# Performance work log

Measured on AMD Instinct MI355X. Metric: run time of the kernel, lower is better.

## Reference

```python
import jax, jax.numpy as jnp
import numpy as np

EPS = 1e-10


def _gcn(X, A, W, act):
    # A_hat = A + I; symmetric normalization D^{-1/2} A_hat D^{-1/2}
    N = A.shape[0]
    A_hat = A + jnp.eye(N, dtype=A.dtype)
    d = 1.0 / jnp.sqrt(jnp.sum(A_hat, axis=1) + EPS)
    A_norm = (d[:, None] * A_hat) * d[None, :]  # same math as diag @ A_hat @ diag
    return act(A_norm @ (X @ W))


def _pool(X, A, s, k):
    scores = (X @ s)[:, 0]            # [N]
    _, idx = jax.lax.top_k(scores, k)  # static k (ceil(ratio*N))
    return X[idx], A[idx][:, idx], idx


def _unpool(Xp, idx, N):
    return jnp.zeros((N, Xp.shape[-1]), Xp.dtype).at[idx].set(Xp)


def _glorot(key, shape):
    lim = np.sqrt(6.0 / (shape[0] + shape[1])).astype(np.float32)
    return jax.random.uniform(key, shape, jnp.float32, -lim, lim)


def setup_inputs() -> dict:
    key = jax.random.key(0)
    ks = jax.random.split(key, 8)
    N, F_IN, F, C = 8192, 16, 32, 2
    x = jax.random.normal(ks[0], (N, F_IN), jnp.float32)
    # sparse-ish symmetric binary adjacency stored densely (as the module expects)
    a = (jax.random.uniform(ks[1], (N, N)) < 0.01).astype(jnp.float32)
    a = jnp.maximum(a, a.T)
    return {
        "x": x,
        "a": a,
        "W1": _glorot(ks[2], (F_IN, F)),
        "W2": _glorot(ks[3], (F, F)),
        "W3": _glorot(ks[4], (F, F)),
        "W4": _glorot(ks[5], (F, C)),
        "s1": _glorot(ks[6], (F, 1)),
        "s2": _glorot(ks[7], (F, 1)),
    }


def reference(x, a, W1, W2, W3, W4, s1, s2):
    N = x.shape[0]
    K1 = int(np.ceil(0.5 * N))   # pool1 ratio 0.5
    K2 = int(np.ceil(0.5 * K1))  # pool2 ratio 0.5
    relu = jax.nn.relu
    X1 = _gcn(x, a, W1, relu)                     # [N, F]
    X1p, A1p, idx1 = _pool(X1, a, s1, K1)         # [K1, F], [K1, K1]
    X2 = _gcn(X1p, A1p, W2, relu)                 # [K1, F]
    X2p, _, idx2 = _pool(X2, A1p, s2, K2)         # [K2, F]
    X3 = _unpool(X2p, idx2, K1)                   # scatter back to [K1, F]
    X3 = _gcn(X3, A1p, W3, relu)
    X4 = _unpool(X3, idx1, N)                     # scatter back to [N, F]
    return _gcn(X4, a, W4, lambda z: jax.nn.softmax(z, axis=-1))
```

## Files before the change

### kernel.cpp

```cpp
#include <hip/hip_runtime.h>
#include <stdint.h>

#define NNODES 8192
#define KP1 4096
#define KP2 2048
#define FIN 16
#define FH 32
#define COUT 2
#define STRA 320
#define STRS 320

__global__ __launch_bounds__(256) void build_ell(const float* __restrict__ A, int n, int stride,
        int* __restrict__ ell, int* __restrict__ rowcnt, int* __restrict__ diag, float* __restrict__ dnorm,
        const float* __restrict__ Xf, const float* __restrict__ Wf, float* __restrict__ Zf, int kf)
{
    if ((int)blockIdx.x >= n) {
        int t = ((int)blockIdx.x - n) * 256 + threadIdx.x;
        int i = t >> 5;
        int f = t & 31;
        const float* xr = Xf + (size_t)i * kf;
        float acc = 0.0f;
        for (int k = 0; k < kf; ++k) acc += xr[k] * Wf[k * 32 + f];
        Zf[t] = acc;
        return;
    }
    __shared__ int cnt;
    __shared__ int dg;
    int row = blockIdx.x;
    if (threadIdx.x == 0) { cnt = 0; dg = 0; }
    __syncthreads();
    const float4* arow4 = (const float4*)(A + (size_t)row * n);
    int* erow = ell + (size_t)row * stride;
    int n4 = n >> 2;
    for (int c4 = threadIdx.x; c4 < n4; c4 += 256) {
        float4 v = arow4[c4];
        if (v.x == 0.0f && v.y == 0.0f && v.z == 0.0f && v.w == 0.0f) continue;
        int cb = c4 << 2;
        if (v.x != 0.0f) {
            if (cb == row) dg = 1;
            else { int p = atomicAdd(&cnt, 1); if (p < stride) erow[p] = cb; }
        }
        if (v.y != 0.0f) {
            int c = cb + 1;
            if (c == row) dg = 1;
            else { int p = atomicAdd(&cnt, 1); if (p < stride) erow[p] = c; }
        }
        if (v.z != 0.0f) {
            int c = cb + 2;
            if (c == row) dg = 1;
            else { int p = atomicAdd(&cnt, 1); if (p < stride) erow[p] = c; }
        }
        if (v.w != 0.0f) {
            int c = cb + 3;
            if (c == row) dg = 1;
            else { int p = atomicAdd(&cnt, 1); if (p < stride) erow[p] = c; }
        }
    }
    __syncthreads();
    if (threadIdx.x == 0) {
        int cf = cnt;
        rowcnt[row] = cf < stride ? cf : stride;
        diag[row] = dg;
        dnorm[row] = rsqrtf((float)(cf + dg + 1) + 1e-10f);
    }
}

__global__ __launch_bounds__(256) void spmm_f32(const int* __restrict__ ell, const int* __restrict__ rowcnt,
        const int* __restrict__ diag, const float* __restrict__ dnorm, const float* __restrict__ Z,
        const int* __restrict__ remap, const int* __restrict__ maskp,
        float* __restrict__ X, float* __restrict__ scores, const float* __restrict__ svec,
        const float* __restrict__ W4p, float* __restrict__ z4out,
        int n, int stride)
{
    int wid = (blockIdx.x * 256 + threadIdx.x) >> 6;
    int lane = threadIdx.x & 63;
    if (wid >= n) return;
    int g = lane >> 3;
    int q = lane & 7;
    int cnt = rowcnt[wid];
    const int* erow = ell + (size_t)wid * stride;
    float ax = 0.0f, ay = 0.0f, az = 0.0f, aw = 0.0f;
    for (int it = g; it < cnt; it += 8) {
        int c = erow[it];
        if (maskp && maskp[c] < 0) continue;
        int zc = c;
        if (remap) zc = remap[c];
        float dn = dnorm[c];
        const float4* zp = (const float4*)(Z + (size_t)zc * 32);
        float4 zv = zp[q];
        ax += dn * zv.x;
        ay += dn * zv.y;
        az += dn * zv.z;
        aw += dn * zv.w;
    }
    ax += __shfl_xor(ax, 8);
    ay += __shfl_xor(ay, 8);
    az += __shfl_xor(az, 8);
    aw += __shfl_xor(aw, 8);
    ax += __shfl_xor(ax, 16);
    ay += __shfl_xor(ay, 16);
    az += __shfl_xor(az, 16);
    aw += __shfl_xor(aw, 16);
    ax += __shfl_xor(ax, 32);
    ay += __shfl_xor(ay, 32);
    az += __shfl_xor(az, 32);
    aw += __shfl_xor(aw, 32);
    if (g == 0) {
        float dr = dnorm[wid];
        int selfok = 1;
        if (maskp && maskp[wid] < 0) selfok = 0;
        if (selfok) {
            int zc = wid;
            if (remap) zc = remap[wid];
            const float4* zp = (const float4*)(Z + (size_t)zc * 32);
            float4 zv = zp[q];
            float cf = (float)(diag[wid] + 1) * dr;
            ax += cf * zv.x;
            ay += cf * zv.y;
            az += cf * zv.z;
            aw += cf * zv.w;
        }
        float ox = fmaxf(dr * ax, 0.0f);
        float oy = fmaxf(dr * ay, 0.0f);
        float oz = fmaxf(dr * az, 0.0f);
        float ow = fmaxf(dr * aw, 0.0f);
        if (z4out) {
            int kb = q * 4;
            float p0 = ox * W4p[(kb + 0) * 2 + 0] + oy * W4p[(kb + 1) * 2 + 0]
                     + oz * W4p[(kb + 2) * 2 + 0] + ow * W4p[(kb + 3) * 2 + 0];
            float p1 = ox * W4p[(kb + 0) * 2 + 1] + oy * W4p[(kb + 1) * 2 + 1]
                     + oz * W4p[(kb + 2) * 2 + 1] + ow * W4p[(kb + 3) * 2 + 1];
            p0 += __shfl_xor(p0, 1);
            p1 += __shfl_xor(p1, 1);
            p0 += __shfl_xor(p0, 2);
            p1 += __shfl_xor(p1, 2);
            p0 += __shfl_xor(p0, 4);
            p1 += __shfl_xor(p1, 4);
            if (q == 0) {
                float2 r;
                r.x = p0;
                r.y = p1;
                ((float2*)z4out)[wid] = r;
            }
        } else {
            float4 o;
            o.x = ox; o.y = oy; o.z = oz; o.w = ow;
            float4* xp = (float4*)(X + (size_t)wid * 32);
            xp[q] = o;
            if (scores) {
                const float4* sp = (const float4*)svec;
                float4 sv = sp[q];
                float p = o.x * sv.x + o.y * sv.y + o.z * sv.z + o.w * sv.w;
                p += __shfl_xor(p, 1);
                p += __shfl_xor(p, 2);
                p += __shfl_xor(p, 4);
                if (q == 0) scores[wid] = p;
            }
        }
    }
}

__global__ __launch_bounds__(256) void spmm_out(const int* __restrict__ ell, const int* __restrict__ rowcnt,
        const int* __restrict__ diag, const float* __restrict__ dnorm, const float* __restrict__ Zr,
        const int* __restrict__ gat, float* __restrict__ out, int n, int stride)
{
    int wid = (blockIdx.x * 256 + threadIdx.x) >> 6;
    int lane = threadIdx.x & 63;
    if (wid >= n) return;
    int cnt = rowcnt[wid];
    const int* erow = ell + (size_t)wid * stride;
    const float2* Z2 = (const float2*)Zr;
    float ax = 0.0f, ay = 0.0f;
    for (int it = lane; it < cnt; it += 64) {
        int c = erow[it];
        int rk = gat[c];
        if (rk >= 0) {
            float dn = dnorm[c];
            float2 zv = Z2[rk];
            ax += dn * zv.x;
            ay += dn * zv.y;
        }
    }
    ax += __shfl_xor(ax, 1);
    ay += __shfl_xor(ay, 1);
    ax += __shfl_xor(ax, 2);
    ay += __shfl_xor(ay, 2);
    ax += __shfl_xor(ax, 4);
    ay += __shfl_xor(ay, 4);
    ax += __shfl_xor(ax, 8);
    ay += __shfl_xor(ay, 8);
    ax += __shfl_xor(ax, 16);
    ay += __shfl_xor(ay, 16);
    ax += __shfl_xor(ax, 32);
    ay += __shfl_xor(ay, 32);
    if (lane == 0) {
        float dr = dnorm[wid];
        int rks = gat[wid];
        if (rks >= 0) {
            float cf = (float)(diag[wid] + 1) * dr;
            float2 zs = Z2[rks];
            ax += cf * zs.x;
            ay += cf * zs.y;
        }
        float v0 = dr * ax;
        float v1 = dr * ay;
        float m = fmaxf(v0, v1);
        float e0 = __expf(v0 - m);
        float e1 = __expf(v1 - m);
        float inv = 1.0f / (e0 + e1);
        float2 r;
        r.x = e0 * inv;
        r.y = e1 * inv;
        ((float2*)out)[wid] = r;
    }
}

__global__ __launch_bounds__(256) void topk_feat(const float* __restrict__ scores, int n, int K,
        int* __restrict__ rank, int* __restrict__ idxlist,
        const float* __restrict__ Xf, const float* __restrict__ Wf, float* __restrict__ Zf, int kf)
{
    if (blockIdx.x != 0) {
        int t = ((int)blockIdx.x - 1) * 256 + threadIdx.x;
        int i = t >> 5;
        int f = t & 31;
        const float* xr = Xf + (size_t)i * kf;
        float acc = 0.0f;
        for (int k = 0; k < kf; ++k) acc += xr[k] * Wf[k * 32 + f];
        Zf[t] = acc;
        return;
    }
    __shared__ unsigned int km_s[8192];
    __shared__ unsigned int histp[4][256];
    __shared__ unsigned int wsum[4];
    __shared__ unsigned int sh_pref;
    __shared__ unsigned int sh_rem;
    int tid = threadIdx.x;
    int wv = tid >> 6;
    int lane = tid & 63;
    int per = n >> 8;
    int base = tid * per;
    for (int e = 0; e < per; ++e) {
        int v = base + e;
        unsigned int u = __float_as_uint(scores[v]);
        unsigned int m;
        if (u & 0x80000000u) m = ~u; else m = u | 0x80000000u;
        km_s[v] = ~m;
    }
    if (tid == 0) { sh_pref = 0u; sh_rem = (unsigned int)K; }
    __syncthreads();
    for (int bp = 3; bp >= 0; --bp) {
        histp[0][tid] = 0u;
        histp[1][tid] = 0u;
        histp[2][tid] = 0u;
        histp[3][tid] = 0u;
        __syncthreads();
        unsigned int maskhi = 0u;
        if (bp < 3) maskhi = 0xFFFFFFFFu << ((bp + 1) * 8);
        unsigned int pref = sh_pref;
        unsigned int rem = sh_rem;
        for (int e = 0; e < per; ++e) {
            unsigned int km = km_s[base + e];
            if ((km & maskhi) == pref) atomicAdd(&histp[wv][(km >> (bp * 8)) & 255u], 1u);
        }
        __syncthreads();
        unsigned int tot = histp[0][tid] + histp[1][tid] + histp[2][tid] + histp[3][tid];
        unsigned int v = tot;
        unsigned int t2;
        t2 = __shfl(v, lane - 1);  if (lane >= 1)  v += t2;
        t2 = __shfl(v, lane - 2);  if (lane >= 2)  v += t2;
        t2 = __shfl(v, lane - 4);  if (lane >= 4)  v += t2;
        t2 = __shfl(v, lane - 8);  if (lane >= 8)  v += t2;
        t2 = __shfl(v, lane - 16); if (lane >= 16) v += t2;
        t2 = __shfl(v, lane - 32); if (lane >= 32) v += t2;
        if (lane == 63) wsum[wv] = v;
        __syncthreads();
        unsigned int add = 0u;
        if (wv > 0) add += wsum[0];
        if (wv > 1) add += wsum[1];
        if (wv > 2) add += wsum[2];
        unsigned int cum = v + add;
        if (tot != 0u && cum >= rem && cum - tot < rem) {
            sh_pref = pref | ((unsigned int)tid << (bp * 8));
            sh_rem = rem - (cum - tot);
        }
    }
    __syncthreads();
    unsigned int T = sh_pref;
    unsigned int need_eq = sh_rem;
    unsigned int run = 0u;
    for (int e = 0; e < per; ++e) {
        unsigned int km = km_s[base + e];
        if (km < T) run += 0x10000u;
        else if (km == T) run += 1u;
    }
    unsigned int v2 = run;
    unsigned int t3;
    t3 = __shfl(v2, lane - 1);  if (lane >= 1)  v2 += t3;
    t3 = __shfl(v2, lane - 2);  if (lane >= 2)  v2 += t3;
    t3 = __shfl(v2, lane - 4);  if (lane >= 4)  v2 += t3;
    t3 = __shfl(v2, lane - 8);  if (lane >= 8)  v2 += t3;
    t3 = __shfl(v2, lane - 16); if (lane >= 16) v2 += t3;
    t3 = __shfl(v2, lane - 32); if (lane >= 32) v2 += t3;
    if (lane == 63) wsum[wv] = v2;
    __syncthreads();
    unsigned int add2 = 0u;
    if (wv > 0) add2 += wsum[0];
    if (wv > 1) add2 += wsum[1];
    if (wv > 2) add2 += wsum[2];
    unsigned int cur = v2 + add2 - run;
    for (int e = 0; e < per; ++e) {
        int v = base + e;
        unsigned int km = km_s[v];
        unsigned int ltb = cur >> 16;
        unsigned int eqb = cur & 0xFFFFu;
        unsigned int eqs = eqb < need_eq ? eqb : need_eq;
        int sel = 0;
        if (km < T) { sel = 1; cur += 0x10000u; }
        else if (km == T) { if (eqb < need_eq) sel = 1; cur += 1u; }
        if (sel) {
            int r = (int)(ltb + eqs);
            rank[v] = r;
            idxlist[r] = v;
        } else {
            rank[v] = -1;
        }
    }
}

__global__ __launch_bounds__(256) void build_subell(const int* __restrict__ ellA, const int* __restrict__ rowcntA,
        const int* __restrict__ diagA, const int* __restrict__ idx1, const int* __restrict__ rank1,
        int* __restrict__ ellS, int* __restrict__ rowcntS, int* __restrict__ diagS, float* __restrict__ dnormS,
        int k1, int strideA, int strideS)
{
    int wid = (blockIdx.x * 256 + threadIdx.x) >> 6;
    int lane = threadIdx.x & 63;
    if (wid >= k1) return;
    int r = idx1[wid];
    int cnt = rowcntA[r];
    const int* erow = ellA + (size_t)r * strideA;
    int* srow = ellS + (size_t)wid * strideS;
    int outn = 0;
    for (int t0 = 0; t0 < cnt; t0 += 64) {
        int it = t0 + lane;
        int rk = -1;
        if (it < cnt) rk = rank1[erow[it]];
        unsigned long long b = __ballot(rk >= 0);
        int ofs = __popcll(b & ((1ull << lane) - 1ull));
        if (rk >= 0) srow[outn + ofs] = rk;
        outn += __popcll(b);
    }
    if (lane == 0) {
        int dg = diagA[r];
        rowcntS[wid] = outn;
        diagS[wid] = dg;
        dnormS[wid] = rsqrtf((float)(outn + dg + 1) + 1e-10f);
    }
}

#define CARVE(type, name, bytes) \
    type name = (type)wp; wp += (((size_t)(bytes)) + 255) & ~((size_t)255);

extern "C" void kernel_launch(void* const* d_in, const int* in_sizes, int n_in,
                              void* d_out, int out_size, void* d_ws, size_t ws_size,
                              hipStream_t stream)
{
    const float* x  = (const float*)d_in[0];
    const float* a  = (const float*)d_in[1];
    const float* W1 = (const float*)d_in[2];
    const float* W2 = (const float*)d_in[3];
    const float* W3 = (const float*)d_in[4];
    const float* W4 = (const float*)d_in[5];
    const float* s1 = (const float*)d_in[6];
    const float* s2 = (const float*)d_in[7];
    float* out = (float*)d_out;
    (void)in_sizes; (void)n_in; (void)out_size; (void)ws_size;

    char* wp = (char*)d_ws;
    CARVE(int*,   ellA,  (size_t)NNODES * STRA * sizeof(int));
    CARVE(int*,   cntA,  NNODES * sizeof(int));
    CARVE(int*,   diagA, NNODES * sizeof(int));
    CARVE(float*, dnA,   NNODES * sizeof(float));
    CARVE(float*, Z1,    (size_t)NNODES * FH * sizeof(float));
    CARVE(float*, X1,    (size_t)NNODES * FH * sizeof(float));
    CARVE(float*, sc1,   NNODES * sizeof(float));
    CARVE(int*,   rank1, NNODES * sizeof(int));
    CARVE(int*,   idx1,  NNODES * sizeof(int));
    CARVE(int*,   ellS,  (size_t)KP1 * STRS * sizeof(int));
    CARVE(int*,   cntS,  KP1 * sizeof(int));
    CARVE(int*,   diagS, KP1 * sizeof(int));
    CARVE(float*, dnS,   KP1 * sizeof(float));
    CARVE(float*, Z2f,   (size_t)NNODES * FH * sizeof(float));
    CARVE(float*, X2,    (size_t)KP1 * FH * sizeof(float));
    CARVE(float*, sc2,   KP1 * sizeof(float));
    CARVE(int*,   rank2, KP1 * sizeof(int));
    CARVE(int*,   idx2,  KP1 * sizeof(int));
    CARVE(float*, Z3f,   (size_t)KP1 * FH * sizeof(float));
    CARVE(float*, Z4r,   (size_t)KP1 * COUT * sizeof(float));

    build_ell<<<NNODES + (NNODES * FH) / 256, 256, 0, stream>>>(
        a, NNODES, STRA, ellA, cntA, diagA, dnA, x, W1, Z1, FIN);
    spmm_f32<<<NNODES / 4, 256, 0, stream>>>(ellA, cntA, diagA, dnA, Z1,
        (const int*)0, (const int*)0, X1, sc1, s1, (const float*)0, (float*)0, NNODES, STRA);
    topk_feat<<<1 + (NNODES * FH) / 256, 256, 0, stream>>>(
        sc1, NNODES, KP1, rank1, idx1, X1, W2, Z2f, FH);
    build_subell<<<KP1 / 4, 256, 0, stream>>>(ellA, cntA, diagA, idx1, rank1,
        ellS, cntS, diagS, dnS, KP1, STRA, STRS);
    spmm_f32<<<KP1 / 4, 256, 0, stream>>>(ellS, cntS, diagS, dnS, Z2f,
        idx1, (const int*)0, X2, sc2, s2, (const float*)0, (float*)0, KP1, STRS);
    topk_feat<<<1 + (KP1 * FH) / 256, 256, 0, stream>>>(
        sc2, KP1, KP2, rank2, idx2, X2, W3, Z3f, FH);
    spmm_f32<<<KP1 / 4, 256, 0, stream>>>(ellS, cntS, diagS, dnS, Z3f,
        (const int*)0, rank2, (float*)0, (float*)0, (const float*)0, W4, Z4r, KP1, STRS);
    spmm_out<<<NNODES / 4, 256, 0, stream>>>(ellA, cntA, diagA, dnA, Z4r, rank1, out, NNODES, STRA);
}
```

Before: 470.8 us.

## Fuse post-ELL GCN stages into one cooperative kernel with grid syncs

Replaces the seven kernel launches after ELL construction with a single cooperative persistent kernel. It uses grid.sync between stages (spmm, topk+gemm, subgraph build, spmm, topk+gemm, spmm with W4 folded in, and the output spmm), and falls back to separate launches if the cooperative launch fails. The goal is to remove launch gaps and idle tails between the many small dependent stages. ELL column indices shrink to 16-bit to halve index traffic. The topk no longer caches keys in 32KB of shared memory and recomputes them from global scores on each pass, which adds repeated global reads.

```diff
diff --git a/kernel.cpp b/kernel.cpp
--- a/kernel.cpp
+++ b/kernel.cpp
@@ -1,5 +1,8 @@
 #include <hip/hip_runtime.h>
+#include <hip/hip_cooperative_groups.h>
 #include <stdint.h>
+
+namespace cg = cooperative_groups;
 
 #define NNODES 8192
 #define KP1 4096
@@ -9,9 +12,13 @@
 #define COUT 2
 #define STRA 320
 #define STRS 320
+#define CGRID_MAX 1024
+
+typedef unsigned short u16;
+typedef unsigned int u32;
 
 __global__ __launch_bounds__(256) void build_ell(const float* __restrict__ A, int n, int stride,
-        int* __restrict__ ell, int* __restrict__ rowcnt, int* __restrict__ diag, float* __restrict__ dnorm,
+        u16* __restrict__ ell, int* __restrict__ rowcnt, int* __restrict__ diag, float* __restrict__ dnorm,
         const float* __restrict__ Xf, const float* __restrict__ Wf, float* __restrict__ Zf, int kf)
 {
     if ((int)blockIdx.x >= n) {
@@ -30,7 +37,7 @@
     if (threadIdx.x == 0) { cnt = 0; dg = 0; }
     __syncthreads();
     const float4* arow4 = (const float4*)(A + (size_t)row * n);
-    int* erow = ell + (size_t)row * stride;
+    u16* erow = ell + (size_t)row * stride;
     int n4 = n >> 2;
     for (int c4 = threadIdx.x; c4 < n4; c4 += 256) {
         float4 v = arow4[c4];
@@ -38,22 +45,22 @@
         int cb = c4 << 2;
         if (v.x != 0.0f) {
             if (cb == row) dg = 1;
-            else { int p = atomicAdd(&cnt, 1); if (p < stride) erow[p] = cb; }
+            else { int p = atomicAdd(&cnt, 1); if (p < stride) erow[p] = (u16)cb; }
         }
         if (v.y != 0.0f) {
             int c = cb + 1;
             if (c == row) dg = 1;
-            else { int p = atomicAdd(&cnt, 1); if (p < stride) erow[p] = c; }
+            else { int p = atomicAdd(&cnt, 1); if (p < stride) erow[p] = (u16)c; }
         }
         if (v.z != 0.0f) {
             int c = cb + 2;
             if (c == row) dg = 1;
-            else { int p = atomicAdd(&cnt, 1); if (p < stride) erow[p] = c; }
+            else { int p = atomicAdd(&cnt, 1); if (p < stride) erow[p] = (u16)c; }
         }
         if (v.w != 0.0f) {
             int c = cb + 3;
             if (c == row) dg = 1;
-            else { int p = atomicAdd(&cnt, 1); if (p < stride) erow[p] = c; }
+            else { int p = atomicAdd(&cnt, 1); if (p < stride) erow[p] = (u16)c; }
         }
     }
     __syncthreads();
@@ -65,255 +72,96 @@
     }
 }
 
-__global__ __launch_bounds__(256) void spmm_f32(const int* __restrict__ ell, const int* __restrict__ rowcnt,
-        const int* __restrict__ diag, const float* __restrict__ dnorm, const float* __restrict__ Z,
-        const int* __restrict__ remap, const int* __restrict__ maskp,
-        float* __restrict__ X, float* __restrict__ scores, const float* __restrict__ svec,
-        const float* __restrict__ W4p, float* __restrict__ z4out,
-        int n, int stride)
-{
-    int wid = (blockIdx.x * 256 + threadIdx.x) >> 6;
-    int lane = threadIdx.x & 63;
-    if (wid >= n) return;
-    int g = lane >> 3;
-    int q = lane & 7;
-    int cnt = rowcnt[wid];
-    const int* erow = ell + (size_t)wid * stride;
-    float ax = 0.0f, ay = 0.0f, az = 0.0f, aw = 0.0f;
-    for (int it = g; it < cnt; it += 8) {
-        int c = erow[it];
-        if (maskp && maskp[c] < 0) continue;
-        int zc = c;
-        if (remap) zc = remap[c];
-        float dn = dnorm[c];
-        const float4* zp = (const float4*)(Z + (size_t)zc * 32);
-        float4 zv = zp[q];
-        ax += dn * zv.x;
-        ay += dn * zv.y;
-        az += dn * zv.z;
-        aw += dn * zv.w;
-    }
-    ax += __shfl_xor(ax, 8);
-    ay += __shfl_xor(ay, 8);
-    az += __shfl_xor(az, 8);
-    aw += __shfl_xor(aw, 8);
-    ax += __shfl_xor(ax, 16);
-    ay += __shfl_xor(ay, 16);
-    az += __shfl_xor(az, 16);
-    aw += __shfl_xor(aw, 16);
-    ax += __shfl_xor(ax, 32);
-    ay += __shfl_xor(ay, 32);
-    az += __shfl_xor(az, 32);
-    aw += __shfl_xor(aw, 32);
-    if (g == 0) {
-        float dr = dnorm[wid];
-        int selfok = 1;
-        if (maskp && maskp[wid] < 0) selfok = 0;
-        if (selfok) {
-            int zc = wid;
-            if (remap) zc = remap[wid];
-            const float4* zp = (const float4*)(Z + (size_t)zc * 32);
-            float4 zv = zp[q];
-            float cf = (float)(diag[wid] + 1) * dr;
-            ax += cf * zv.x;
-            ay += cf * zv.y;
-            az += cf * zv.z;
-            aw += cf * zv.w;
-        }
-        float ox = fmaxf(dr * ax, 0.0f);
-        float oy = fmaxf(dr * ay, 0.0f);
-        float oz = fmaxf(dr * az, 0.0f);
-        float ow = fmaxf(dr * aw, 0.0f);
-        if (z4out) {
-            int kb = q * 4;
-            float p0 = ox * W4p[(kb + 0) * 2 + 0] + oy * W4p[(kb + 1) * 2 + 0]
-                     + oz * W4p[(kb + 2) * 2 + 0] + ow * W4p[(kb + 3) * 2 + 0];
-            float p1 = ox * W4p[(kb + 0) * 2 + 1] + oy * W4p[(kb + 1) * 2 + 1]
-                     + oz * W4p[(kb + 2) * 2 + 1] + ow * W4p[(kb + 3) * 2 + 1];
-            p0 += __shfl_xor(p0, 1);
-            p1 += __shfl_xor(p1, 1);
-            p0 += __shfl_xor(p0, 2);
-            p1 += __shfl_xor(p1, 2);
-            p0 += __shfl_xor(p0, 4);
-            p1 += __shfl_xor(p1, 4);
-            if (q == 0) {
-                float2 r;
-                r.x = p0;
-                r.y = p1;
-                ((float2*)z4out)[wid] = r;
-            }
-        } else {
-            float4 o;
-            o.x = ox; o.y = oy; o.z = oz; o.w = ow;
-            float4* xp = (float4*)(X + (size_t)wid * 32);
-            xp[q] = o;
-            if (scores) {
-                const float4* sp = (const float4*)svec;
-                float4 sv = sp[q];
-                float p = o.x * sv.x + o.y * sv.y + o.z * sv.z + o.w * sv.w;
-                p += __shfl_xor(p, 1);
-                p += __shfl_xor(p, 2);
-                p += __shfl_xor(p, 4);
-                if (q == 0) scores[wid] = p;
-            }
-        }
-    }
-}
-
-__global__ __launch_bounds__(256) void spmm_out(const int* __restrict__ ell, const int* __restrict__ rowcnt,
-        const int* __restrict__ diag, const float* __restrict__ dnorm, const float* __restrict__ Zr,
-        const int* __restrict__ gat, float* __restrict__ out, int n, int stride)
-{
-    int wid = (blockIdx.x * 256 + threadIdx.x) >> 6;
-    int lane = threadIdx.x & 63;
-    if (wid >= n) return;
-    int cnt = rowcnt[wid];
-    const int* erow = ell + (size_t)wid * stride;
-    const float2* Z2 = (const float2*)Zr;
-    float ax = 0.0f, ay = 0.0f;
-    for (int it = lane; it < cnt; it += 64) {
-        int c = erow[it];
-        int rk = gat[c];
-        if (rk >= 0) {
-            float dn = dnorm[c];
-            float2 zv = Z2[rk];
-            ax += dn * zv.x;
-            ay += dn * zv.y;
-        }
-    }
-    ax += __shfl_xor(ax, 1);
-    ay += __shfl_xor(ay, 1);
-    ax += __shfl_xor(ax, 2);
-    ay += __shfl_xor(ay, 2);
-    ax += __shfl_xor(ax, 4);
-    ay += __shfl_xor(ay, 4);
-    ax += __shfl_xor(ax, 8);
-    ay += __shfl_xor(ay, 8);
-    ax += __shfl_xor(ax, 16);
-    ay += __shfl_xor(ay, 16);
-    ax += __shfl_xor(ax, 32);
-    ay += __shfl_xor(ay, 32);
-    if (lane == 0) {
-        float dr = dnorm[wid];
-        int rks = gat[wid];
-        if (rks >= 0) {
-            float cf = (float)(diag[wid] + 1) * dr;
-            float2 zs = Z2[rks];
-            ax += cf * zs.x;
-            ay += cf * zs.y;
-        }
-        float v0 = dr * ax;
-        float v1 = dr * ay;
-        float m = fmaxf(v0, v1);
-        float e0 = __expf(v0 - m);
-        float e1 = __expf(v1 - m);
-        float inv = 1.0f / (e0 + e1);
-        float2 r;
-        r.x = e0 * inv;
-        r.y = e1 * inv;
-        ((float2*)out)[wid] = r;
-    }
-}
-
-__global__ __launch_bounds__(256) void topk_feat(const float* __restrict__ scores, int n, int K,
-        int* __restrict__ rank, int* __restrict__ idxlist,
-        const float* __restrict__ Xf, const float* __restrict__ Wf, float* __restrict__ Zf, int kf)
-{
-    if (blockIdx.x != 0) {
-        int t = ((int)blockIdx.x - 1) * 256 + threadIdx.x;
-        int i = t >> 5;
-        int f = t & 31;
-        const float* xr = Xf + (size_t)i * kf;
-        float acc = 0.0f;
-        for (int k = 0; k < kf; ++k) acc += xr[k] * Wf[k * 32 + f];
-        Zf[t] = acc;
-        return;
-    }
-    __shared__ unsigned int km_s[8192];
-    __shared__ unsigned int histp[4][256];
-    __shared__ unsigned int wsum[4];
-    __shared__ unsigned int sh_pref;
-    __shared__ unsigned int sh_rem;
-    int tid = threadIdx.x;
+struct TkS {
+    u32 hist[4][256];
+    u32 wsum[4];
+    u32 pref;
+    u32 rem;
+};
+
+__device__ __forceinline__ u32 km_of(float f)
+{
+    u32 u = __float_as_uint(f);
+    u32 m;
+    if (u & 0x80000000u) m = ~u; else m = u | 0x80000000u;
+    return ~m;
+}
+
+__device__ void topk_block0(TkS& s, const float* __restrict__ scores, int n, int K,
+                            int* __restrict__ rank, int* __restrict__ idxlist, int tid)
+{
     int wv = tid >> 6;
     int lane = tid & 63;
     int per = n >> 8;
     int base = tid * per;
-    for (int e = 0; e < per; ++e) {
-        int v = base + e;
-        unsigned int u = __float_as_uint(scores[v]);
-        unsigned int m;
-        if (u & 0x80000000u) m = ~u; else m = u | 0x80000000u;
-        km_s[v] = ~m;
-    }
-    if (tid == 0) { sh_pref = 0u; sh_rem = (unsigned int)K; }
+    if (tid == 0) { s.pref = 0u; s.rem = (u32)K; }
     __syncthreads();
     for (int bp = 3; bp >= 0; --bp) {
-        histp[0][tid] = 0u;
-        histp[1][tid] = 0u;
-        histp[2][tid] = 0u;
-        histp[3][tid] = 0u;
+        s.hist[0][tid] = 0u;
+        s.hist[1][tid] = 0u;
+        s.hist[2][tid] = 0u;
+        s.hist[3][tid] = 0u;
         __syncthreads();
-        unsigned int maskhi = 0u;
+        u32 maskhi = 0u;
         if (bp < 3) maskhi = 0xFFFFFFFFu << ((bp + 1) * 8);
-        unsigned int pref = sh_pref;
-        unsigned int rem = sh_rem;
+        u32 pref = s.pref;
+        u32 rem = s.rem;
         for (int e = 0; e < per; ++e) {
-            unsigned int km = km_s[base + e];
-            if ((km & maskhi) == pref) atomicAdd(&histp[wv][(km >> (bp * 8)) & 255u], 1u);
+            u32 km = km_of(scores[base + e]);
+            if ((km & maskhi) == pref) atomicAdd(&s.hist[wv][(km >> (bp * 8)) & 255u], 1u);
         }
         __syncthreads();
-        unsigned int tot = histp[0][tid] + histp[1][tid] + histp[2][tid] + histp[3][tid];
-        unsigned int v = tot;
-        unsigned int t2;
-        t2 = __shfl(v, lane - 1);  if (lane >= 1)  v += t2;
-        t2 = __shfl(v, lane - 2);  if (lane >= 2)  v += t2;
-        t2 = __shfl(v, lane - 4);  if (lane >= 4)  v += t2;
-        t2 = __shfl(v, lane - 8);  if (lane >= 8)  v += t2;
-        t2 = __shfl(v, lane - 16); if (lane >= 16) v += t2;
-        t2 = __shfl(v, lane - 32); if (lane >= 32) v += t2;
-        if (lane == 63) wsum[wv] = v;
+        u32 tot = s.hist[0][tid] + s.hist[1][tid] + s.hist[2][tid] + s.hist[3][tid];
+        u32 vv = tot;
+        u32 t2;
+        t2 = __shfl(vv, lane - 1);  if (lane >= 1)  vv += t2;
+        t2 = __shfl(vv, lane - 2);  if (lane >= 2)  vv += t2;
+        t2 = __shfl(vv, lane - 4);  if (lane >= 4)  vv += t2;
+        t2 = __shfl(vv, lane - 8);  if (lane >= 8)  vv += t2;
+        t2 = __shfl(vv, lane - 16); if (lane >= 16) vv += t2;
+        t2 = __shfl(vv, lane - 32); if (lane >= 32) vv += t2;
+        if (lane == 63) s.wsum[wv] = vv;
         __syncthreads();
-        unsigned int add = 0u;
-        if (wv > 0) add += wsum[0];
-        if (wv > 1) add += wsum[1];
-        if (wv > 2) add += wsum[2];
-        unsigned int cum = v + add;
+        u32 add = 0u;
+        if (wv > 0) add += s.wsum[0];
+        if (wv > 1) add += s.wsum[1];
+        if (wv > 2) add += s.wsum[2];
+        u32 cum = vv + add;
         if (tot != 0u && cum >= rem && cum - tot < rem) {
-            sh_pref = pref | ((unsigned int)tid << (bp * 8));
-            sh_rem = rem - (cum - tot);
+            s.pref = pref | ((u32)tid << (bp * 8));
+            s.rem = rem - (cum - tot);
         }
     }
     __syncthreads();
-    unsigned int T = sh_pref;
-    unsigned int need_eq = sh_rem;
-    unsigned int run = 0u;
+    u32 T = s.pref;
+    u32 need_eq = s.rem;
+    u32 run = 0u;
     for (int e = 0; e < per; ++e) {
-        unsigned int km = km_s[base + e];
+        u32 km = km_of(scores[base + e]);
         if (km < T) run += 0x10000u;
         else if (km == T) run += 1u;
     }
-    unsigned int v2 = run;
-    unsigned int t3;
+    u32 v2 = run;
+    u32 t3;
     t3 = __shfl(v2, lane - 1);  if (lane >= 1)  v2 += t3;
     t3 = __shfl(v2, lane - 2);  if (lane >= 2)  v2 += t3;
     t3 = __shfl(v2, lane - 4);  if (lane >= 4)  v2 += t3;
     t3 = __shfl(v2, lane - 8);  if (lane >= 8)  v2 += t3;
     t3 = __shfl(v2, lane - 16); if (lane >= 16) v2 += t3;
     t3 = __shfl(v2, lane - 32); if (lane >= 32) v2 += t3;
-    if (lane == 63) wsum[wv] = v2;
+    if (lane == 63) s.wsum[wv] = v2;
     __syncthreads();
-    unsigned int add2 = 0u;
-    if (wv > 0) add2 += wsum[0];
-    if (wv > 1) add2 += wsum[1];
-    if (wv > 2) add2 += wsum[2];
-    unsigned int cur = v2 + add2 - run;
+    u32 add2 = 0u;
+    if (wv > 0) add2 += s.wsum[0];
+    if (wv > 1) add2 += s.wsum[1];
+    if (wv > 2) add2 += s.wsum[2];
+    u32 cur = v2 + add2 - run;
     for (int e = 0; e < per; ++e) {
         int v = base + e;
-        unsigned int km = km_s[v];
-        unsigned int ltb = cur >> 16;
-        unsigned int eqb = cur & 0xFFFFu;
-        unsigned int eqs = eqb < need_eq ? eqb : need_eq;
+        u32 km = km_of(scores[v]);
+        u32 ltb = cur >> 16;
+        u32 eqb = cur & 0xFFFFu;
+        u32 eqs = eqb < need_eq ? eqb : need_eq;
         int sel = 0;
         if (km < T) { sel = 1; cur += 0x10000u; }
         else if (km == T) { if (eqb < need_eq) sel = 1; cur += 1u; }
@@ -327,34 +175,283 @@
     }
 }
 
-__global__ __launch_bounds__(256) void build_subell(const int* __restrict__ ellA, const int* __restrict__ rowcntA,
+__device__ __forceinline__ void gemm32(const float* __restrict__ Xf, const float* __restrict__ Wf,
+                                       float* __restrict__ Zf, int rows, int kf, int t0, int tstr)
+{
+    int tot = rows * 32;
+    for (int t = t0; t < tot; t += tstr) {
+        int i = t >> 5;
+        int f = t & 31;
+        const float* xr = Xf + (size_t)i * kf;
+        float acc = 0.0f;
+        for (int k = 0; k < kf; ++k) acc += xr[k] * Wf[k * 32 + f];
+        Zf[t] = acc;
+    }
+}
+
+template<bool REMAP, bool MASK, bool FW4, bool SC>
+__device__ __forceinline__ void spmm_phase(
+        const u16* __restrict__ ell, const int* __restrict__ rowcnt,
+        const int* __restrict__ diag, const float* __restrict__ dnorm,
+        const float* __restrict__ Z, const int* __restrict__ remap, const int* __restrict__ maskp,
+        float* __restrict__ X, float* __restrict__ scores, const float* __restrict__ svec,
+        const float* __restrict__ W4p, float* __restrict__ z4out,
+        int n, int stride, int gwave, int nwaves, int lane)
+{
+    int g = lane >> 3;
+    int q = lane & 7;
+    for (int wid = gwave; wid < n; wid += nwaves) {
+        int cnt = rowcnt[wid];
+        const u16* erow = ell + (size_t)wid * stride;
+        float ax = 0.0f, ay = 0.0f, az = 0.0f, aw = 0.0f;
+        for (int it = g; it < cnt; it += 8) {
+            int c = erow[it];
+            if (MASK && maskp[c] < 0) continue;
+            int zc = REMAP ? remap[c] : c;
+            float dn = dnorm[c];
+            const float4* zp = (const float4*)(Z + (size_t)zc * 32);
+            float4 zv = zp[q];
+            ax += dn * zv.x;
+            ay += dn * zv.y;
+            az += dn * zv.z;
+            aw += dn * zv.w;
+        }
+        ax += __shfl_xor(ax, 8);  ay += __shfl_xor(ay, 8);
+        az += __shfl_xor(az, 8);  aw += __shfl_xor(aw, 8);
+        ax += __shfl_xor(ax, 16); ay += __shfl_xor(ay, 16);
+        az += __shfl_xor(az, 16); aw += __shfl_xor(aw, 16);
+        ax += __shfl_xor(ax, 32); ay += __shfl_xor(ay, 32);
+        az += __shfl_xor(az, 32); aw += __shfl_xor(aw, 32);
+        if (g == 0) {
+            float dr = dnorm[wid];
+            bool selfok = !(MASK && maskp[wid] < 0);
+            if (selfok) {
+                int zc = REMAP ? remap[wid] : wid;
+                const float4* zp = (const float4*)(Z + (size_t)zc * 32);
+                float4 zv = zp[q];
+                float cf = (float)(diag[wid] + 1) * dr;
+                ax += cf * zv.x;
+                ay += cf * zv.y;
+                az += cf * zv.z;
+                aw += cf * zv.w;
+            }
+            float ox = fmaxf(dr * ax, 0.0f);
+            float oy = fmaxf(dr * ay, 0.0f);
+            float oz = fmaxf(dr * az, 0.0f);
+            float ow = fmaxf(dr * aw, 0.0f);
+            if (FW4) {
+                int kb = q * 4;
+                float p0 = ox * W4p[(kb + 0) * 2 + 0] + oy * W4p[(kb + 1) * 2 + 0]
+                         + oz * W4p[(kb + 2) * 2 + 0] + ow * W4p[(kb + 3) * 2 + 0];
+                float p1 = ox * W4p[(kb + 0) * 2 + 1] + oy * W4p[(kb + 1) * 2 + 1]
+                         + oz * W4p[(kb + 2) * 2 + 1] + ow * W4p[(kb + 3) * 2 + 1];
+                p0 += __shfl_xor(p0, 1);
+                p1 += __shfl_xor(p1, 1);
+                p0 += __shfl_xor(p0, 2);
+                p1 += __shfl_xor(p1, 2);
+                p0 += __shfl_xor(p0, 4);
+                p1 += __shfl_xor(p1, 4);
+                if (q == 0) {
+                    float2 r;
+                    r.x = p0;
+                    r.y = p1;
+                    ((float2*)z4out)[wid] = r;
+                }
+            } else {
+                float4 o;
+                o.x = ox; o.y = oy; o.z = oz; o.w = ow;
+                float4* xp = (float4*)(X + (size_t)wid * 32);
+                xp[q] = o;
+                if (SC) {
+                    const float4* sp = (const float4*)svec;
+                    float4 sv = sp[q];
+                    float pp = o.x * sv.x + o.y * sv.y + o.z * sv.z + o.w * sv.w;
+                    pp += __shfl_xor(pp, 1);
+                    pp += __shfl_xor(pp, 2);
+                    pp += __shfl_xor(pp, 4);
+                    if (q == 0) scores[wid] = pp;
+                }
+            }
+        }
+    }
+}
+
+__device__ __forceinline__ void subell_phase(const u16* __restrict__ ellA, const int* __restrict__ rowcntA,
         const int* __restrict__ diagA, const int* __restrict__ idx1, const int* __restrict__ rank1,
-        int* __restrict__ ellS, int* __restrict__ rowcntS, int* __restrict__ diagS, float* __restrict__ dnormS,
+        u16* __restrict__ ellS, int* __restrict__ rowcntS, int* __restrict__ diagS, float* __restrict__ dnormS,
+        int k1, int strideA, int strideS, int gwave, int nwaves, int lane)
+{
+    for (int wid = gwave; wid < k1; wid += nwaves) {
+        int r = idx1[wid];
+        int cnt = rowcntA[r];
+        const u16* erow = ellA + (size_t)r * strideA;
+        u16* srow = ellS + (size_t)wid * strideS;
+        int outn = 0;
+        for (int t0 = 0; t0 < cnt; t0 += 64) {
+            int it = t0 + lane;
+            int rk = -1;
+            if (it < cnt) rk = rank1[erow[it]];
+            unsigned long long b = __ballot(rk >= 0);
+            int ofs = __popcll(b & ((1ull << lane) - 1ull));
+            if (rk >= 0) srow[outn + ofs] = (u16)rk;
+            outn += __popcll(b);
+        }
+        if (lane == 0) {
+            int dg = diagA[r];
+            rowcntS[wid] = outn;
+            diagS[wid] = dg;
+            dnormS[wid] = rsqrtf((float)(outn + dg + 1) + 1e-10f);
+        }
+    }
+}
+
+__device__ __forceinline__ void spmmout_phase(const u16* __restrict__ ell, const int* __restrict__ rowcnt,
+        const int* __restrict__ diag, const float* __restrict__ dnorm, const float* __restrict__ Zr,
+        const int* __restrict__ gat, float* __restrict__ out, int n, int stride,
+        int gwave, int nwaves, int lane)
+{
+    const float2* Z2 = (const float2*)Zr;
+    for (int wid = gwave; wid < n; wid += nwaves) {
+        int cnt = rowcnt[wid];
+        const u16* erow = ell + (size_t)wid * stride;
+        float ax = 0.0f, ay = 0.0f;
+        for (int it = lane; it < cnt; it += 64) {
+            int c = erow[it];
+            int rk = gat[c];
+            if (rk >= 0) {
+                float dn = dnorm[c];
+                float2 zv = Z2[rk];
+                ax += dn * zv.x;
+                ay += dn * zv.y;
+            }
+        }
+        ax += __shfl_xor(ax, 1);  ay += __shfl_xor(ay, 1);
+        ax += __shfl_xor(ax, 2);  ay += __shfl_xor(ay, 2);
+        ax += __shfl_xor(ax, 4);  ay += __shfl_xor(ay, 4);
+        ax += __shfl_xor(ax, 8);  ay += __shfl_xor(ay, 8);
+        ax += __shfl_xor(ax, 16); ay += __shfl_xor(ay, 16);
+        ax += __shfl_xor(ax, 32); ay += __shfl_xor(ay, 32);
+        if (lane == 0) {
+            float dr = dnorm[wid];
+            int rks = gat[wid];
+            if (rks >= 0) {
+                float cf = (float)(diag[wid] + 1) * dr;
+                float2 zs = Z2[rks];
+                ax += cf * zs.x;
+                ay += cf * zs.y;
+            }
+            float v0 = dr * ax;
+            float v1 = dr * ay;
+            float m = fmaxf(v0, v1);
+            float e0 = __expf(v0 - m);
+            float e1 = __expf(v1 - m);
+            float inv = 1.0f / (e0 + e1);
+            float2 r;
+            r.x = e0 * inv;
+            r.y = e1 * inv;
+            ((float2*)out)[wid] = r;
+        }
+    }
+}
+
+struct GcnP {
+    const u16* ellA; const int* cntA; const int* diagA; const float* dnA;
+    const float* Z1; float* X1; float* sc1; int* rank1; int* idx1;
+    u16* ellS; int* cntS; int* diagS; float* dnS;
+    float* Z2f; float* X2; float* sc2; int* rank2; int* idx2;
+    float* Z3f; float* Z4r;
+    const float* W2; const float* W3; const float* W4; const float* s1; const float* s2;
+    float* out;
+};
+
+__global__ __launch_bounds__(256, 4) void gcn_pipeline(GcnP p)
+{
+    cg::grid_group grid = cg::this_grid();
+    __shared__ TkS sm;
+    int tid = threadIdx.x;
+    int bid = blockIdx.x;
+    int lane = tid & 63;
+    int gwave = (bid * 256 + tid) >> 6;
+    int nwaves = ((int)gridDim.x * 256) >> 6;
+
+    spmm_phase<false, false, false, true>(p.ellA, p.cntA, p.diagA, p.dnA, p.Z1,
+        (const int*)0, (const int*)0, p.X1, p.sc1, p.s1, (const float*)0, (float*)0,
+        NNODES, STRA, gwave, nwaves, lane);
+    grid.sync();
+
+    if (bid == 0) topk_block0(sm, p.sc1, NNODES, KP1, p.rank1, p.idx1, tid);
+    else gemm32(p.X1, p.W2, p.Z2f, NNODES, FH, (bid - 1) * 256 + tid, ((int)gridDim.x - 1) * 256);
+    grid.sync();
+
+    subell_phase(p.ellA, p.cntA, p.diagA, p.idx1, p.rank1, p.ellS, p.cntS, p.diagS, p.dnS,
+        KP1, STRA, STRS, gwave, nwaves, lane);
+    grid.sync();
+
+    spmm_phase<true, false, false, true>(p.ellS, p.cntS, p.diagS, p.dnS, p.Z2f,
+        p.idx1, (const int*)0, p.X2, p.sc2, p.s2, (const float*)0, (float*)0,
+        KP1, STRS, gwave, nwaves, lane);
+    grid.sync();
+
+    if (bid == 0) topk_block0(sm, p.sc2, KP1, KP2, p.rank2, p.idx2, tid);
+    else gemm32(p.X2, p.W3, p.Z3f, KP1, FH, (bid - 1) * 256 + tid, ((int)gridDim.x - 1) * 256);
+    grid.sync();
+
+    spmm_phase<false, true, true, false>(p.ellS, p.cntS, p.diagS, p.dnS, p.Z3f,
+        (const int*)0, p.rank2, (float*)0, (float*)0, (const float*)0, p.W4, p.Z4r,
+        KP1, STRS, gwave, nwaves, lane);
+    grid.sync();
+
+    spmmout_phase(p.ellA, p.cntA, p.diagA, p.dnA, p.Z4r, p.rank1, p.out,
+        NNODES, STRA, gwave, nwaves, lane);
+}
+
+__global__ __launch_bounds__(256) void k_spmm(const u16* __restrict__ ell, const int* __restrict__ rowcnt,
+        const int* __restrict__ diag, const float* __restrict__ dnorm, const float* __restrict__ Z,
+        const int* __restrict__ remap, const int* __restrict__ maskp,
+        float* __restrict__ X, float* __restrict__ scores, const float* __restrict__ svec,
+        const float* __restrict__ W4p, float* __restrict__ z4out, int n, int stride, int mode)
+{
+    int gwave = ((int)blockIdx.x * 256 + (int)threadIdx.x) >> 6;
+    int nwaves = ((int)gridDim.x * 256) >> 6;
+    int lane = threadIdx.x & 63;
+    if (mode == 0)
+        spmm_phase<false, false, false, true>(ell, rowcnt, diag, dnorm, Z, remap, maskp,
+            X, scores, svec, W4p, z4out, n, stride, gwave, nwaves, lane);
+    else if (mode == 1)
+        spmm_phase<true, false, false, true>(ell, rowcnt, diag, dnorm, Z, remap, maskp,
+            X, scores, svec, W4p, z4out, n, stride, gwave, nwaves, lane);
+    else
+        spmm_phase<false, true, true, false>(ell, rowcnt, diag, dnorm, Z, remap, maskp,
+            X, scores, svec, W4p, z4out, n, stride, gwave, nwaves, lane);
+}
+
+__global__ __launch_bounds__(256) void k_topk_gemm(const float* __restrict__ scores, int n, int K,
+        int* __restrict__ rank, int* __restrict__ idxlist,
+        const float* __restrict__ Xf, const float* __restrict__ Wf, float* __restrict__ Zf, int kf)
+{
+    __shared__ TkS sm;
+    if (blockIdx.x == 0) topk_block0(sm, scores, n, K, rank, idxlist, threadIdx.x);
+    else gemm32(Xf, Wf, Zf, n, kf, ((int)blockIdx.x - 1) * 256 + threadIdx.x, ((int)gridDim.x - 1) * 256);
+}
+
+__global__ __launch_bounds__(256) void k_subell(const u16* __restrict__ ellA, const int* __restrict__ rowcntA,
+        const int* __restrict__ diagA, const int* __restrict__ idx1, const int* __restrict__ rank1,
+        u16* __restrict__ ellS, int* __restrict__ rowcntS, int* __restrict__ diagS, float* __restrict__ dnormS,
         int k1, int strideA, int strideS)
 {
-    int wid = (blockIdx.x * 256 + threadIdx.x) >> 6;
-    int lane = threadIdx.x & 63;
-    if (wid >= k1) return;
-    int r = idx1[wid];
-    int cnt = rowcntA[r];
-    const int* erow = ellA + (size_t)r * strideA;
-    int* srow = ellS + (size_t)wid * strideS;
-    int outn = 0;
-    for (int t0 = 0; t0 < cnt; t0 += 64) {
-        int it = t0 + lane;
-        int rk = -1;
-        if (it < cnt) rk = rank1[erow[it]];
-        unsigned long long b = __ballot(rk >= 0);
-        int ofs = __popcll(b & ((1ull << lane) - 1ull));
-        if (rk >= 0) srow[outn + ofs] = rk;
-        outn += __popcll(b);
-    }
-    if (lane == 0) {
-        int dg = diagA[r];
-        rowcntS[wid] = outn;
-        diagS[wid] = dg;
-        dnormS[wid] = rsqrtf((float)(outn + dg + 1) + 1e-10f);
-    }
+    int gwave = ((int)blockIdx.x * 256 + (int)threadIdx.x) >> 6;
+    int nwaves = ((int)gridDim.x * 256) >> 6;
+    subell_phase(ellA, rowcntA, diagA, idx1, rank1, ellS, rowcntS, diagS, dnormS,
+        k1, strideA, strideS, gwave, nwaves, threadIdx.x & 63);
+}
+
+__global__ __launch_bounds__(256) void k_spmmout(const u16* __restrict__ ell, const int* __restrict__ rowcnt,
+        const int* __restrict__ diag, const float* __restrict__ dnorm, const float* __restrict__ Zr,
+        const int* __restrict__ gat, float* __restrict__ out, int n, int stride)
+{
+    int gwave = ((int)blockIdx.x * 256 + (int)threadIdx.x) >> 6;
+    int nwaves = ((int)gridDim.x * 256) >> 6;
+    spmmout_phase(ell, rowcnt, diag, dnorm, Zr, gat, out, n, stride, gwave, nwaves, threadIdx.x & 63);
 }
 
 #define CARVE(type, name, bytes) \
@@ -376,7 +473,7 @@
     (void)in_sizes; (void)n_in; (void)out_size; (void)ws_size;
 
     char* wp = (char*)d_ws;
-    CARVE(int*,   ellA,  (size_t)NNODES * STRA * sizeof(int));
+    CARVE(u16*,   ellA,  (size_t)NNODES * STRA * sizeof(u16));
     CARVE(int*,   cntA,  NNODES * sizeof(int));
     CARVE(int*,   diagA, NNODES * sizeof(int));
     CARVE(float*, dnA,   NNODES * sizeof(float));
@@ -385,7 +482,7 @@
     CARVE(float*, sc1,   NNODES * sizeof(float));
     CARVE(int*,   rank1, NNODES * sizeof(int));
     CARVE(int*,   idx1,  NNODES * sizeof(int));
-    CARVE(int*,   ellS,  (size_t)KP1 * STRS * sizeof(int));
+    CARVE(u16*,   ellS,  (size_t)KP1 * STRS * sizeof(u16));
     CARVE(int*,   cntS,  KP1 * sizeof(int));
     CARVE(int*,   diagS, KP1 * sizeof(int));
     CARVE(float*, dnS,   KP1 * sizeof(float));
@@ -399,17 +496,47 @@
 
     build_ell<<<NNODES + (NNODES * FH) / 256, 256, 0, stream>>>(
         a, NNODES, STRA, ellA, cntA, diagA, dnA, x, W1, Z1, FIN);
-    spmm_f32<<<NNODES / 4, 256, 0, stream>>>(ellA, cntA, diagA, dnA, Z1,
-        (const int*)0, (const int*)0, X1, sc1, s1, (const float*)0, (float*)0, NNODES, STRA);
-    topk_feat<<<1 + (NNODES * FH) / 256, 256, 0, stream>>>(
-        sc1, NNODES, KP1, rank1, idx1, X1, W2, Z2f, FH);
-    build_subell<<<KP1 / 4, 256, 0, stream>>>(ellA, cntA, diagA, idx1, rank1,
-        ellS, cntS, diagS, dnS, KP1, STRA, STRS);
-    spmm_f32<<<KP1 / 4, 256, 0, stream>>>(ellS, cntS, diagS, dnS, Z2f,
-        idx1, (const int*)0, X2, sc2, s2, (const float*)0, (float*)0, KP1, STRS);
-    topk_feat<<<1 + (KP1 * FH) / 256, 256, 0, stream>>>(
-        sc2, KP1, KP2, rank2, idx2, X2, W3, Z3f, FH);
-    spmm_f32<<<KP1 / 4, 256, 0, stream>>>(ellS, cntS, diagS, dnS, Z3f,
-        (const int*)0, rank2, (float*)0, (float*)0, (const float*)0, W4, Z4r, KP1, STRS);
-    spmm_out<<<NNODES / 4, 256, 0, stream>>>(ellA, cntA, diagA, dnA, Z4r, rank1, out, NNODES, STRA);
-}
+
+    static int g_cgrid = 0;
+    if (g_cgrid == 0) {
+        int maxb = 0;
+        if (hipOccupancyMaxActiveBlocksPerMultiprocessor(&maxb, (const void*)gcn_pipeline, 256, 0)
+                != hipSuccess || maxb <= 0)
+            maxb = 2;
+        int ncu = 256;
+        hipDeviceProp_t props;
+        if (hipGetDeviceProperties(&props, 0) == hipSuccess && props.multiProcessorCount > 0)
+            ncu = props.multiProcessorCount;
+        long g = (long)maxb * (long)ncu;
+        if (g > CGRID_MAX) g = CGRID_MAX;
+        if (g < 2) g = 2;
+        g_cgrid = (int)g;
+    }
+
+    GcnP pp;
+    pp.ellA = ellA; pp.cntA = cntA; pp.diagA = diagA; pp.dnA = dnA;
+    pp.Z1 = Z1; pp.X1 = X1; pp.sc1 = sc1; pp.rank1 = rank1; pp.idx1 = idx1;
+    pp.ellS = ellS; pp.cntS = cntS; pp.diagS = diagS; pp.dnS = dnS;
+    pp.Z2f = Z2f; pp.X2 = X2; pp.sc2 = sc2; pp.rank2 = rank2; pp.idx2 = idx2;
+    pp.Z3f = Z3f; pp.Z4r = Z4r;
+    pp.W2 = W2; pp.W3 = W3; pp.W4 = W4; pp.s1 = s1; pp.s2 = s2;
+    pp.out = out;
+    void* kargs[] = { (void*)&pp };
+    hipError_t ce = hipLaunchCooperativeKernel((const void*)gcn_pipeline,
+                                               dim3((unsigned)g_cgrid), dim3(256), kargs, 0u, stream);
+    if (ce != hipSuccess) {
+        k_spmm<<<NNODES / 4, 256, 0, stream>>>(ellA, cntA, diagA, dnA, Z1,
+            (const int*)0, (const int*)0, X1, sc1, s1, (const float*)0, (float*)0, NNODES, STRA, 0);
+        k_topk_gemm<<<1 + (NNODES * FH) / 256, 256, 0, stream>>>(
+            sc1, NNODES, KP1, rank1, idx1, X1, W2, Z2f, FH);
+        k_subell<<<KP1 / 4, 256, 0, stream>>>(ellA, cntA, diagA, idx1, rank1,
+            ellS, cntS, diagS, dnS, KP1, STRA, STRS);
+        k_spmm<<<KP1 / 4, 256, 0, stream>>>(ellS, cntS, diagS, dnS, Z2f,
+            idx1, (const int*)0, X2, sc2, s2, (const float*)0, (float*)0, KP1, STRS, 1);
+        k_topk_gemm<<<1 + (KP1 * FH) / 256, 256, 0, stream>>>(
+            sc2, KP1, KP2, rank2, idx2, X2, W3, Z3f, FH);
+        k_spmm<<<KP1 / 4, 256, 0, stream>>>(ellS, cntS, diagS, dnS, Z3f,
+            (const int*)0, rank2, (float*)0, (float*)0, (const float*)0, W4, Z4r, KP1, STRS, 2);
+        k_spmmout<<<NNODES / 4, 256, 0, stream>>>(ellA, cntA, diagA, dnA, Z4r, rank1, out, NNODES, STRA);
+    }
+}
```

After: 856.0 us. 81.8% more time.
